# Optimization experiments

Measured on AMD Instinct MI355X. Metric: run time of the kernel, lower is better.

The kernel has to match this reference:

```python
import jax, jax.numpy as jnp
import numpy as np

WIN = 7
K1, K2 = 0.01, 0.03


def _box_filter(x, w):
    """Valid-padding uniform box filter. x: (B, D, H, W); w: (1, 1, k, k)."""
    B, D, H, Wd = x.shape
    k = w.shape[-1]
    y = jax.lax.conv_general_dilated(
        x.reshape(B * D, 1, H, Wd), w, window_strides=(1, 1), padding='VALID',
        dimension_numbers=('NCHW', 'OIHW', 'NCHW'))
    return y.reshape(B, D, H - k + 1, Wd - k + 1)


def setup_inputs() -> dict:
    key = jax.random.key(0)
    kx, ky = jax.random.split(key)
    X = jax.random.uniform(kx, (4, 64, 256, 256), dtype=jnp.float32)
    Y = jax.random.uniform(ky, (4, 64, 256, 256), dtype=jnp.float32)
    w = jnp.ones((1, 1, WIN, WIN), dtype=jnp.float32) / (WIN * WIN)  # buffer self.w
    return {"X": X, "Y": Y, "w": w}


def reference(X, Y, w):
    data_range = 1.0
    C1 = (K1 * data_range) ** 2
    C2 = (K2 * data_range) ** 2
    NP = WIN * WIN
    cov_norm = NP / (NP - 1)

    ux = _box_filter(X, w)
    uy = _box_filter(Y, w)
    uxx = _box_filter(X * X, w)
    uyy = _box_filter(Y * Y, w)
    uxy = _box_filter(X * Y, w)

    vx = cov_norm * (uxx - ux * ux)
    vy = cov_norm * (uyy - uy * uy)
    vxy = cov_norm * (uxy - ux * uy)

    A1 = 2.0 * ux * uy + C1
    A2 = 2.0 * vxy + C2
    B1 = ux * ux + uy * uy + C1
    B2 = vx + vy + C2
    S = (A1 * A2) / (B1 * B2)  # (B, D, H', W')

    # Faithful to torch: ssim_per_slice[:, i] = S_i.mean() (mean over batch AND spatial),
    # then 1 - mean over depth, returned per batch element.
    slice_means = S.mean(axis=(0, 2, 3))  # (D,)
    loss = 1.0 - slice_means.mean()
    return jnp.full((X.shape[0],), loss, dtype=X.dtype)
```

## Files before the change

kernel.cpp:

```cpp
#include <hip/hip_runtime.h>

#define H 256
#define W 256
#define W4 (W / 4)
#define OWID 250
#define NIMG 256
#define BAND 10
#define NBANDS 25
#define NBLK (NBANDS * NIMG)
#define RIN 16
#define WPB 4
#define NBLOCKS (NBLK / WPB)

__device__ __forceinline__ float4 f4zero() { return make_float4(0.f, 0.f, 0.f, 0.f); }

__global__ __launch_bounds__(256) void ssim_band_kernel(
    const float* __restrict__ X, const float* __restrict__ Y,
    float* __restrict__ partial)
{
    const int lane = threadIdx.x & 63;
    const int wid  = blockIdx.x * WPB + (threadIdx.x >> 6);
    const int img  = wid / NBANDS;
    const int band = wid % NBANDS;
    const int r0 = band * BAND;

    const float4* Xp = (const float4*)X + ((size_t)img * H + r0) * W4 + lane;
    const float4* Yp = (const float4*)Y + ((size_t)img * H + r0) * W4 + lane;

    float4 sx = f4zero(), sy = f4zero(), sxy = f4zero(), spp = f4zero();

    float4 px[2], py[2], ox[2], oy[2];
    px[0] = Xp[0];      py[0] = Yp[0];
    px[1] = Xp[W4];     py[1] = Yp[W4];

    const float C1  = 1e-4f;
    const float C2  = 9e-4f;
    const float AA  = 1.f / 2401.f;
    const float C2A = 2.f / 2401.f;
    const float T1  = 1.f / 24.f;
    const float T2  = -1.f / 1176.f;
    const float T3  = 1.f / 48.f;
    const float T4  = -1.f / 2352.f;
    float lsum = 0.0f;

    #pragma unroll
    for (int r = 0; r < RIN; ++r) {
        const float4 xn = px[r & 1], yn = py[r & 1];
        if (r + 2 < RIN) {
            px[r & 1] = Xp[(r + 2) * W4];
            py[r & 1] = Yp[(r + 2) * W4];
        }
        float4 xo = f4zero(), yo = f4zero();
        if (r >= 7) { xo = ox[r & 1]; yo = oy[r & 1]; }
        if (r >= 5 && r <= RIN - 3) {
            ox[r & 1] = Xp[(r - 5) * W4];
            oy[r & 1] = Yp[(r - 5) * W4];
        }

        if (r < 6) {
            sx.x += xn.x; sx.y += xn.y; sx.z += xn.z; sx.w += xn.w;
            sy.x += yn.x; sy.y += yn.y; sy.z += yn.z; sy.w += yn.w;
            sxy.x = fmaf(xn.x, yn.x, sxy.x);
            sxy.y = fmaf(xn.y, yn.y, sxy.y);
            sxy.z = fmaf(xn.z, yn.z, sxy.z);
            sxy.w = fmaf(xn.w, yn.w, sxy.w);
            spp.x = fmaf(xn.x, xn.x, fmaf(yn.x, yn.x, spp.x));
            spp.y = fmaf(xn.y, xn.y, fmaf(yn.y, yn.y, spp.y));
            spp.z = fmaf(xn.z, xn.z, fmaf(yn.z, yn.z, spp.z));
            spp.w = fmaf(xn.w, xn.w, fmaf(yn.w, yn.w, spp.w));
        } else {
            sx.x += xn.x - xo.x; sx.y += xn.y - xo.y;
            sx.z += xn.z - xo.z; sx.w += xn.w - xo.w;
            sy.x += yn.x - yo.x; sy.y += yn.y - yo.y;
            sy.z += yn.z - yo.z; sy.w += yn.w - yo.w;
            sxy.x = fmaf(xn.x, yn.x, fmaf(-xo.x, yo.x, sxy.x));
            sxy.y = fmaf(xn.y, yn.y, fmaf(-xo.y, yo.y, sxy.y));
            sxy.z = fmaf(xn.z, yn.z, fmaf(-xo.z, yo.z, sxy.z));
            sxy.w = fmaf(xn.w, yn.w, fmaf(-xo.w, yo.w, sxy.w));
            spp.x = fmaf(xn.x, xn.x, fmaf(yn.x, yn.x, fmaf(-xo.x, xo.x, fmaf(-yo.x, yo.x, spp.x))));
            spp.y = fmaf(xn.y, xn.y, fmaf(yn.y, yn.y, fmaf(-xo.y, xo.y, fmaf(-yo.y, yo.y, spp.y))));
            spp.z = fmaf(xn.z, xn.z, fmaf(yn.z, yn.z, fmaf(-xo.z, xo.z, fmaf(-yo.z, yo.z, spp.z))));
            spp.w = fmaf(xn.w, xn.w, fmaf(yn.w, yn.w, fmaf(-xo.w, xo.w, fmaf(-yo.w, yo.w, spp.w))));

            float wx[4], wy[4], wpp[4], wxy[4];
            #define HWIN(S, WA)                                            \
            {                                                              \
                const float bx = __shfl_down(S.x, 1);                      \
                const float by = __shfl_down(S.y, 1);                      \
                const float bz = __shfl_down(S.z, 1);                      \
                const float bw = __shfl_down(S.w, 1);                      \
                const float cx = __shfl_down(S.x, 2);                      \
                const float cy = __shfl_down(S.y, 2);                      \
                WA[0] = S.x + S.y + S.z + S.w + bx + by + bz;              \
                WA[1] = WA[0] - S.x + bw;                                  \
                WA[2] = WA[1] - S.y + cx;                                  \
                WA[3] = WA[2] - S.z + cy;                                  \
            }
            HWIN(sx,  wx)
            HWIN(sy,  wy)
            HWIN(spp, wpp)
            HWIN(sxy, wxy)
            #undef HWIN

            #pragma unroll
            for (int s = 0; s < 4; ++s) {
                const float P  = wx[s] * wy[s];
                const float Qs = fmaf(wy[s], wy[s], wx[s] * wx[s]);
                const float A1 = fmaf(C2A, P, C1);
                const float B1 = fmaf(AA, Qs, C1);
                const float A2 = fmaf(T1, wxy[s], fmaf(T2, P, C2));
                const float B2 = fmaf(T3, wpp[s], fmaf(T4, Qs, C2));
                const float S  = (A1 * A2) * __builtin_amdgcn_rcpf(B1 * B2);
                if (4 * lane + s < OWID) lsum += S;
            }
        }
    }

    #pragma unroll
    for (int off = 32; off > 0; off >>= 1)
        lsum += __shfl_down(lsum, off, 64);
    if (lane == 0) partial[wid] = lsum;
}

__global__ __launch_bounds__(256) void ssim_reduce_kernel(
    const float* __restrict__ partial, float* __restrict__ out)
{
    const int tid = threadIdx.x;
    double acc = 0.0;
    for (int i = tid; i < NBLK; i += 256)
        acc += (double)partial[i];
    #pragma unroll
    for (int off = 32; off > 0; off >>= 1)
        acc += __shfl_down(acc, off, 64);
    __shared__ double wsumd[4];
    if ((tid & 63) == 0) wsumd[tid >> 6] = acc;
    __syncthreads();
    if (tid == 0) {
        double total = wsumd[0] + wsumd[1] + wsumd[2] + wsumd[3];
        float loss = (float)(1.0 - total / 16000000.0);
        out[0] = loss; out[1] = loss; out[2] = loss; out[3] = loss;
    }
}

extern "C" void kernel_launch(void* const* d_in, const int* in_sizes, int n_in,
                              void* d_out, int out_size, void* d_ws, size_t ws_size,
                              hipStream_t stream) {
    const float* X = (const float*)d_in[0];
    const float* Y = (const float*)d_in[1];
    float* out = (float*)d_out;
    float* partial = (float*)d_ws;

    hipLaunchKernelGGL(ssim_band_kernel, dim3(NBLOCKS), dim3(256), 0, stream,
                       X, Y, partial);
    hipLaunchKernelGGL(ssim_reduce_kernel, dim3(1), dim3(256), 0, stream,
                       partial, out);
}
```

Before: 159.4 us.

## Process two images per wavefront with interleaved row streams

```diff
diff --git a/kernel.cpp b/kernel.cpp
--- a/kernel.cpp
+++ b/kernel.cpp
@@ -7,119 +7,148 @@
 #define NIMG 256
 #define BAND 10
 #define NBANDS 25
-#define NBLK (NBANDS * NIMG)
+#define NPAIR 3200
+#define WPB 4
+#define NBLOCKS (NPAIR / WPB)
 #define RIN 16
-#define WPB 4
-#define NBLOCKS (NBLK / WPB)
+
 
 __device__ __forceinline__ float4 f4zero() { return make_float4(0.f, 0.f, 0.f, 0.f); }
+
+#define CC1 1e-4f
+#define CC2 9e-4f
+#define KAA (1.f / 2401.f)
+#define K2A (2.f / 2401.f)
+#define KT1 (1.f / 24.f)
+#define KT2 (-1.f / 1176.f)
+#define KT3 (1.f / 48.f)
+#define KT4 (-1.f / 2352.f)
+
+struct Stream {
+    const float4* Xp;
+    const float4* Yp;
+    float4 sx, sy, sxy, spp;
+    float4 px0, py0, px1, py1;
+    float4 ox0, oy0, ox1, oy1;
+};
+
+__device__ __forceinline__ void s_init(Stream& s, const float* X, const float* Y,
+                                       int img, int band, int lane) {
+    const int r0 = band * BAND;
+    s.Xp = (const float4*)X + ((size_t)img * H + r0) * W4 + lane;
+    s.Yp = (const float4*)Y + ((size_t)img * H + r0) * W4 + lane;
+    s.sx = f4zero(); s.sy = f4zero(); s.sxy = f4zero(); s.spp = f4zero();
+    s.px0 = s.Xp[0];  s.py0 = s.Yp[0];
+    s.px1 = s.Xp[W4]; s.py1 = s.Yp[W4];
+}
+
+template<int R>
+__device__ __forceinline__ void s_row(Stream& s, const float4 xn, const float4 yn,
+                                      const float4 xo, const float4 yo,
+                                      const int lane, float& lsum) {
+    s.sx.x += xn.x - xo.x; s.sx.y += xn.y - xo.y;
+    s.sx.z += xn.z - xo.z; s.sx.w += xn.w - xo.w;
+    s.sy.x += yn.x - yo.x; s.sy.y += yn.y - yo.y;
+    s.sy.z += yn.z - yo.z; s.sy.w += yn.w - yo.w;
+    s.sxy.x = fmaf(xn.x, yn.x, fmaf(-xo.x, yo.x, s.sxy.x));
+    s.sxy.y = fmaf(xn.y, yn.y, fmaf(-xo.y, yo.y, s.sxy.y));
+    s.sxy.z = fmaf(xn.z, yn.z, fmaf(-xo.z, yo.z, s.sxy.z));
+    s.sxy.w = fmaf(xn.w, yn.w, fmaf(-xo.w, yo.w, s.sxy.w));
+    s.spp.x = fmaf(xn.x, xn.x, fmaf(yn.x, yn.x, fmaf(-xo.x, xo.x, fmaf(-yo.x, yo.x, s.spp.x))));
+    s.spp.y = fmaf(xn.y, xn.y, fmaf(yn.y, yn.y, fmaf(-xo.y, xo.y, fmaf(-yo.y, yo.y, s.spp.y))));
+    s.spp.z = fmaf(xn.z, xn.z, fmaf(yn.z, yn.z, fmaf(-xo.z, xo.z, fmaf(-yo.z, yo.z, s.spp.z))));
+    s.spp.w = fmaf(xn.w, xn.w, fmaf(yn.w, yn.w, fmaf(-xo.w, xo.w, fmaf(-yo.w, yo.w, s.spp.w))));
+
+    if constexpr (R >= 6) {
+        float wx[4], wy[4], wpp[4], wxy[4];
+        #define HWIN(S, WA)                                                  \
+        {                                                                    \
+            const float bx = __shfl_down(S.x, 1);                            \
+            const float by = __shfl_down(S.y, 1);                            \
+            const float bz = __shfl_down(S.z, 1);                            \
+            const float bw = __shfl_down(S.w, 1);                            \
+            const float cx = __shfl_down(S.x, 2);                            \
+            const float cy = __shfl_down(S.y, 2);                            \
+            WA[0] = S.x + S.y + S.z + S.w + bx + by + bz;                    \
+            WA[1] = WA[0] - S.x + bw;                                        \
+            WA[2] = WA[1] - S.y + cx;                                        \
+            WA[3] = WA[2] - S.z + cy;                                        \
+        }
+        HWIN(s.sx,  wx)
+        HWIN(s.sy,  wy)
+        HWIN(s.spp, wpp)
+        HWIN(s.sxy, wxy)
+        #undef HWIN
+        #pragma unroll
+        for (int c = 0; c < 4; ++c) {
+            const float P  = wx[c] * wy[c];
+            const float Qs = fmaf(wy[c], wy[c], wx[c] * wx[c]);
+            const float A1 = fmaf(K2A, P, CC1);
+            const float B1 = fmaf(KAA, Qs, CC1);
+            const float A2 = fmaf(KT1, wxy[c], fmaf(KT2, P, CC2));
+            const float B2 = fmaf(KT3, wpp[c], fmaf(KT4, Qs, CC2));
+            const float S  = (A1 * A2) * __builtin_amdgcn_rcpf(B1 * B2);
+            if (4 * lane + c < OWID) lsum += S;
+        }
+    }
+}
+
+template<int R>
+__device__ __forceinline__ void stepPair(Stream& a, Stream& b,
+                                         const int lane, float& lsum) {
+    const float4 xnA = (R & 1) ? a.px1 : a.px0;
+    const float4 ynA = (R & 1) ? a.py1 : a.py0;
+    const float4 xnB = (R & 1) ? b.px1 : b.px0;
+    const float4 ynB = (R & 1) ? b.py1 : b.py0;
+    float4 xoA = f4zero(), yoA = f4zero(), xoB = f4zero(), yoB = f4zero();
+    if constexpr (R >= 7) {
+        xoA = (R & 1) ? a.ox1 : a.ox0;  yoA = (R & 1) ? a.oy1 : a.oy0;
+        xoB = (R & 1) ? b.ox1 : b.ox0;  yoB = (R & 1) ? b.oy1 : b.oy0;
+    }
+    if constexpr (R + 2 < RIN) {
+        if constexpr (R & 1) {
+            a.px1 = a.Xp[(R + 2) * W4]; a.py1 = a.Yp[(R + 2) * W4];
+            b.px1 = b.Xp[(R + 2) * W4]; b.py1 = b.Yp[(R + 2) * W4];
+        } else {
+            a.px0 = a.Xp[(R + 2) * W4]; a.py0 = a.Yp[(R + 2) * W4];
+            b.px0 = b.Xp[(R + 2) * W4]; b.py0 = b.Yp[(R + 2) * W4];
+        }
+    }
+    if constexpr (R >= 5 && R + 2 <= RIN - 1) {
+        if constexpr (R & 1) {
+            a.ox1 = a.Xp[(R - 5) * W4]; a.oy1 = a.Yp[(R - 5) * W4];
+            b.ox1 = b.Xp[(R - 5) * W4]; b.oy1 = b.Yp[(R - 5) * W4];
+        } else {
+            a.ox0 = a.Xp[(R - 5) * W4]; a.oy0 = a.Yp[(R - 5) * W4];
+            b.ox0 = b.Xp[(R - 5) * W4]; b.oy0 = b.Yp[(R - 5) * W4];
+        }
+    }
+    s_row<R>(a, xnA, ynA, xoA, yoA, lane, lsum);
+    s_row<R>(b, xnB, ynB, xoB, yoB, lane, lsum);
+    if constexpr (R + 1 < RIN) stepPair<R + 1>(a, b, lane, lsum);
+}
 
 __global__ __launch_bounds__(256) void ssim_band_kernel(
     const float* __restrict__ X, const float* __restrict__ Y,
     float* __restrict__ partial)
 {
     const int lane = threadIdx.x & 63;
-    const int wid  = blockIdx.x * WPB + (threadIdx.x >> 6);
-    const int img  = wid / NBANDS;
-    const int band = wid % NBANDS;
-    const int r0 = band * BAND;
+    const int w    = blockIdx.x * WPB + (threadIdx.x >> 6);
+    const int imgA  = w / NBANDS;
+    const int band  = w % NBANDS;
+    const int imgB  = imgA + 128;
 
-    const float4* Xp = (const float4*)X + ((size_t)img * H + r0) * W4 + lane;
-    const float4* Yp = (const float4*)Y + ((size_t)img * H + r0) * W4 + lane;
+    Stream a, b;
+    s_init(a, X, Y, imgA, band, lane);
+    s_init(b, X, Y, imgB, band, lane);
 
-    float4 sx = f4zero(), sy = f4zero(), sxy = f4zero(), spp = f4zero();
-
-    float4 px[2], py[2], ox[2], oy[2];
-    px[0] = Xp[0];      py[0] = Yp[0];
-    px[1] = Xp[W4];     py[1] = Yp[W4];
-
-    const float C1  = 1e-4f;
-    const float C2  = 9e-4f;
-    const float AA  = 1.f / 2401.f;
-    const float C2A = 2.f / 2401.f;
-    const float T1  = 1.f / 24.f;
-    const float T2  = -1.f / 1176.f;
-    const float T3  = 1.f / 48.f;
-    const float T4  = -1.f / 2352.f;
     float lsum = 0.0f;
-
-    #pragma unroll
-    for (int r = 0; r < RIN; ++r) {
-        const float4 xn = px[r & 1], yn = py[r & 1];
-        if (r + 2 < RIN) {
-            px[r & 1] = Xp[(r + 2) * W4];
-            py[r & 1] = Yp[(r + 2) * W4];
-        }
-        float4 xo = f4zero(), yo = f4zero();
-        if (r >= 7) { xo = ox[r & 1]; yo = oy[r & 1]; }
-        if (r >= 5 && r <= RIN - 3) {
-            ox[r & 1] = Xp[(r - 5) * W4];
-            oy[r & 1] = Yp[(r - 5) * W4];
-        }
-
-        if (r < 6) {
-            sx.x += xn.x; sx.y += xn.y; sx.z += xn.z; sx.w += xn.w;
-            sy.x += yn.x; sy.y += yn.y; sy.z += yn.z; sy.w += yn.w;
-            sxy.x = fmaf(xn.x, yn.x, sxy.x);
-            sxy.y = fmaf(xn.y, yn.y, sxy.y);
-            sxy.z = fmaf(xn.z, yn.z, sxy.z);
-            sxy.w = fmaf(xn.w, yn.w, sxy.w);
-            spp.x = fmaf(xn.x, xn.x, fmaf(yn.x, yn.x, spp.x));
-            spp.y = fmaf(xn.y, xn.y, fmaf(yn.y, yn.y, spp.y));
-            spp.z = fmaf(xn.z, xn.z, fmaf(yn.z, yn.z, spp.z));
-            spp.w = fmaf(xn.w, xn.w, fmaf(yn.w, yn.w, spp.w));
-        } else {
-            sx.x += xn.x - xo.x; sx.y += xn.y - xo.y;
-            sx.z += xn.z - xo.z; sx.w += xn.w - xo.w;
-            sy.x += yn.x - yo.x; sy.y += yn.y - yo.y;
-            sy.z += yn.z - yo.z; sy.w += yn.w - yo.w;
-            sxy.x = fmaf(xn.x, yn.x, fmaf(-xo.x, yo.x, sxy.x));
-            sxy.y = fmaf(xn.y, yn.y, fmaf(-xo.y, yo.y, sxy.y));
-            sxy.z = fmaf(xn.z, yn.z, fmaf(-xo.z, yo.z, sxy.z));
-            sxy.w = fmaf(xn.w, yn.w, fmaf(-xo.w, yo.w, sxy.w));
-            spp.x = fmaf(xn.x, xn.x, fmaf(yn.x, yn.x, fmaf(-xo.x, xo.x, fmaf(-yo.x, yo.x, spp.x))));
-            spp.y = fmaf(xn.y, xn.y, fmaf(yn.y, yn.y, fmaf(-xo.y, xo.y, fmaf(-yo.y, yo.y, spp.y))));
-            spp.z = fmaf(xn.z, xn.z, fmaf(yn.z, yn.z, fmaf(-xo.z, xo.z, fmaf(-yo.z, yo.z, spp.z))));
-            spp.w = fmaf(xn.w, xn.w, fmaf(yn.w, yn.w, fmaf(-xo.w, xo.w, fmaf(-yo.w, yo.w, spp.w))));
-
-            float wx[4], wy[4], wpp[4], wxy[4];
-            #define HWIN(S, WA)                                            \
-            {                                                              \
-                const float bx = __shfl_down(S.x, 1);                      \
-                const float by = __shfl_down(S.y, 1);                      \
-                const float bz = __shfl_down(S.z, 1);                      \
-                const float bw = __shfl_down(S.w, 1);                      \
-                const float cx = __shfl_down(S.x, 2);                      \
-                const float cy = __shfl_down(S.y, 2);                      \
-                WA[0] = S.x + S.y + S.z + S.w + bx + by + bz;              \
-                WA[1] = WA[0] - S.x + bw;                                  \
-                WA[2] = WA[1] - S.y + cx;                                  \
-                WA[3] = WA[2] - S.z + cy;                                  \
-            }
-            HWIN(sx,  wx)
-            HWIN(sy,  wy)
-            HWIN(spp, wpp)
-            HWIN(sxy, wxy)
-            #undef HWIN
-
-            #pragma unroll
-            for (int s = 0; s < 4; ++s) {
-                const float P  = wx[s] * wy[s];
-                const float Qs = fmaf(wy[s], wy[s], wx[s] * wx[s]);
-                const float A1 = fmaf(C2A, P, C1);
-                const float B1 = fmaf(AA, Qs, C1);
-                const float A2 = fmaf(T1, wxy[s], fmaf(T2, P, C2));
-                const float B2 = fmaf(T3, wpp[s], fmaf(T4, Qs, C2));
-                const float S  = (A1 * A2) * __builtin_amdgcn_rcpf(B1 * B2);
-                if (4 * lane + s < OWID) lsum += S;
-            }
-        }
-    }
+    stepPair<0>(a, b, lane, lsum);
 
     #pragma unroll
     for (int off = 32; off > 0; off >>= 1)
         lsum += __shfl_down(lsum, off, 64);
-    if (lane == 0) partial[wid] = lsum;
+    if (lane == 0) partial[w] = lsum;
 }
 
 __global__ __launch_bounds__(256) void ssim_reduce_kernel(
@@ -127,7 +156,7 @@
 {
     const int tid = threadIdx.x;
     double acc = 0.0;
-    for (int i = tid; i < NBLK; i += 256)
+    for (int i = tid; i < NPAIR; i += 256)
         acc += (double)partial[i];
     #pragma unroll
     for (int off = 32; off > 0; off >>= 1)
```

After: 166.3 us. 1.04x slower.
